# Optimization experiments

Measured on AMD Instinct MI355X. Metric: run time of the kernel, lower is better.

## Reference

```python
import jax, jax.numpy as jnp
import numpy as np
from jax import lax

EPS = 1e-4

@jax.custom_vjp
def bin_active(x):
    # sign binarization with straight-through estimator
    return jnp.sign(x)

def _bin_fwd(x):
    return jnp.sign(x), x

def _bin_bwd(x, g):
    # grad zeroed where input >= 1 or <= -1 (matches torch ge/le)
    return (g * ((x > -1.0) & (x < 1.0)).astype(g.dtype),)

bin_active.defvjp(_bin_fwd, _bin_bwd)

def setup_inputs() -> dict:
    key = jax.random.key(0)
    k1, k2, k3 = jax.random.split(key, 3)
    x = jax.random.normal(k1, (32, 64, 112, 112), dtype=jnp.float32)
    gamma = jnp.ones((64,), dtype=jnp.float32)
    beta = jnp.zeros((64,), dtype=jnp.float32)
    W = jax.random.normal(k2, (64, 64, 3, 3), dtype=jnp.float32) * 0.05
    b = jax.random.normal(k3, (64,), dtype=jnp.float32) * 0.05
    return {"x": x, "gamma": gamma, "beta": beta, "W": W, "b": b}

def reference(x, gamma, beta, W, b):
    # training-mode BatchNorm2d: per-channel batch stats over (N,H,W), biased var
    mean = jnp.mean(x, axis=(0, 2, 3), keepdims=True)
    var = jnp.mean((x - mean) ** 2, axis=(0, 2, 3), keepdims=True)
    xbn = (x - mean) / jnp.sqrt(var + EPS)
    xbn = xbn * gamma.reshape(1, -1, 1, 1) + beta.reshape(1, -1, 1, 1)
    # sign binarize (abs-channel-mean from BinActive is unused downstream)
    xb = bin_active(xbn)
    # conv2d k=3, s=1, p=1
    y = lax.conv_general_dilated(
        xb, W,
        window_strides=(1, 1),
        padding=((1, 1), (1, 1)),
        dimension_numbers=("NCHW", "OIHW", "NCHW"),
    ) + b.reshape(1, -1, 1, 1)
    return jax.nn.relu(y)
```

## Files before the change

kernel.cpp:

```cpp
#include <hip/hip_runtime.h>
#include <stdint.h>

typedef float    f32x4 __attribute__((ext_vector_type(4)));
typedef int      i32x4 __attribute__((ext_vector_type(4)));
typedef uint32_t u32;

#define NHW 401408.0

__device__ __forceinline__ void gload_lds16(const void* g, void* l) {
  typedef __attribute__((address_space(1))) const u32 gu32;
  typedef __attribute__((address_space(3))) u32 lu32;
  __builtin_amdgcn_global_load_lds((gu32*)g, (lu32*)l, 16, 0, 0);
}

__global__ __launch_bounds__(64) void prep_weights(const float* __restrict__ Wg,
                                                   int8_t* __restrict__ Wq,
                                                   float* __restrict__ sc) {
  int o = blockIdx.x, c = threadIdx.x;
  float w[9]; float m = 0.f;
#pragma unroll
  for (int tap = 0; tap < 9; ++tap) {
    w[tap] = Wg[(o * 64 + c) * 9 + tap];
    m = fmaxf(m, fabsf(w[tap]));
  }
#pragma unroll
  for (int off = 32; off > 0; off >>= 1) m = fmaxf(m, __shfl_xor(m, off));
  float s = m / 127.f;
  float inv = (s > 0.f) ? 1.f / s : 0.f;
  if (c == 0) sc[o] = s;
  int of = o >> 4, m16 = o & 15, kg = c >> 4, j = c & 15;
#pragma unroll
  for (int tap = 0; tap < 9; ++tap) {
    int q = (int)rintf(w[tap] * inv);
    q = q > 127 ? 127 : (q < -127 ? -127 : q);
    Wq[(tap * 4 + of) * 1024 + (kg * 16 + m16) * 16 + j] = (int8_t)q;
  }
}

__global__ __launch_bounds__(256) void stats_kernel(const float* __restrict__ x,
                                                    double* __restrict__ sums) {
  int blk = blockIdx.x;
  const float4* p = (const float4*)(x + (size_t)blk * 12544);
  float s = 0.f, q = 0.f;
  for (int i = threadIdx.x; i < 3136; i += 256) {
    float4 v = p[i];
    s += (v.x + v.y) + (v.z + v.w);
    q += v.x * v.x + v.y * v.y + v.z * v.z + v.w * v.w;
  }
#pragma unroll
  for (int off = 32; off > 0; off >>= 1) {
    s += __shfl_down(s, off);
    q += __shfl_down(q, off);
  }
  __shared__ float ls[8];
  int wv = threadIdx.x >> 6;
  if ((threadIdx.x & 63) == 0) { ls[wv] = s; ls[4 + wv] = q; }
  __syncthreads();
  if (threadIdx.x == 0) {
    double S = (double)ls[0] + ls[1] + ls[2] + ls[3];
    double Q = (double)ls[4] + ls[5] + ls[6] + ls[7];
    int c = blk & 63;
    atomicAdd(&sums[c], S);
    atomicAdd(&sums[64 + c], Q);
  }
}

__global__ void finalize_kernel(const double* __restrict__ sums,
                                const float* __restrict__ gamma,
                                const float* __restrict__ beta,
                                float* __restrict__ ad) {
  int c = threadIdx.x;
  double mean = sums[c] / NHW;
  double var  = sums[64 + c] / NHW - mean * mean;
  double istd = 1.0 / sqrt(var + 1e-4);
  double a = (double)gamma[c] * istd;
  double d = (double)beta[c] - mean * a;
  ad[c]      = (float)a;
  ad[64 + c] = (float)d;
}

__global__ __launch_bounds__(256) void binarize_kernel(const float* __restrict__ x,
                                                       const float* __restrict__ ad,
                                                       u32* __restrict__ signs) {
  __shared__ u32 buf[64 * 29];
  const int n = blockIdx.y, h = blockIdx.x, t = threadIdx.x;
  {
    const int c = t & 63, q = t >> 6;
    const float a_c = ad[c], d_c = ad[64 + c];
    const f32x4* src = (const f32x4*)(x + (size_t)(n * 64 + c) * 12544 + h * 112 + q * 28);
#pragma unroll
    for (int i = 0; i < 7; ++i) {
      f32x4 v = src[i];
      u32 p = 0;
#pragma unroll
      for (int k = 0; k < 4; ++k) {
        float tt = fmaf(v[k], a_c, d_c);
        u32 b = (tt > 0.f) ? 0x01u : ((tt < 0.f) ? 0xFFu : 0x00u);
        p |= b << (8 * k);
      }
      buf[c * 29 + q * 7 + i] = p;
    }
  }
  __syncthreads();
  u32* row = signs + (size_t)(n * 112 + h) * 114 * 16;
  const int cq = t & 15, wg = t >> 4;
  if (t < 16) row[t] = 0;
  else if (t < 32) row[113 * 16 + (t - 16)] = 0;
#pragma unroll
  for (int pass = 0; pass < 7; ++pass) {
    int w = wg + 16 * pass;
    int sh = (w & 3) * 8;
    u32 o = 0;
#pragma unroll
    for (int j = 0; j < 4; ++j) {
      u32 v = buf[(cq * 4 + j) * 29 + (w >> 2)];
      o |= ((v >> sh) & 0xFFu) << (8 * j);
    }
    row[(w + 1) * 16 + cq] = o;
  }
}

#define SROW 7296
__global__ __launch_bounds__(256, 2) void conv_kernel(
    const int8_t* __restrict__ signs, const int8_t* __restrict__ Wq,
    const float* __restrict__ sc, const float* __restrict__ bias,
    float* __restrict__ out) {
  __shared__ __align__(16) char smem[6 * SROW];
  const int tid = threadIdx.x, lane = tid & 63, wv = tid >> 6;
  const int b = (blockIdx.x & 7) * 112 + (blockIdx.x >> 3);
  const int n = b / 28, th = b - n * 28;
  const int h0 = th * 4;

  for (int r = wv; r < 6; r += 4) {
    int gh = h0 - 1 + r;
    char* dst = smem + r * SROW;
    if ((unsigned)gh < 112u) {
      const char* g = (const char*)signs + (size_t)(n * 112 + gh) * SROW;
#pragma unroll
      for (int off = 0; off < 7168; off += 1024)
        gload_lds16(g + off + lane * 16, dst + off);
      if (lane < 8) gload_lds16(g + 7168 + lane * 16, dst + 7168);
    } else {
      uint4 z = {0, 0, 0, 0};
      for (int off = lane * 16; off < SROW; off += 1024) *(uint4*)(dst + off) = z;
    }
  }
  __syncthreads();

  i32x4 acc[4][7] = {};
  const int pw = lane & 15, kg = lane >> 4;
#pragma unroll
  for (int tap = 0; tap < 9; ++tap) {
    const int kh = tap / 3, kw = tap - 3 * kh;
    i32x4 af[4], bf[7];
#pragma unroll
    for (int of = 0; of < 4; ++of)
      af[of] = *(const i32x4*)(Wq + (tap * 4 + of) * 1024 + lane * 16);
#pragma unroll
    for (int wf = 0; wf < 7; ++wf)
      bf[wf] = *(const i32x4*)(smem + ((wv + kh) * 114 + wf * 16 + pw + kw) * 64 + kg * 16);
#pragma unroll
    for (int of = 0; of < 4; ++of)
#pragma unroll
      for (int wf = 0; wf < 7; ++wf)
        acc[of][wf] = __builtin_amdgcn_mfma_i32_16x16x64_i8(af[of], bf[wf],
                                                            acc[of][wf], 0, 0, 0);
  }
  __syncthreads();

  float* patch = (float*)smem + wv * (16 * 114);
  const size_t obase = ((size_t)n * 64) * 12544 + (size_t)(h0 + wv) * 112;
#pragma unroll
  for (int of = 0; of < 4; ++of) {
    float sv[4], bv[4];
#pragma unroll
    for (int r = 0; r < 4; ++r) {
      int o = of * 16 + kg * 4 + r;
      sv[r] = sc[o]; bv[r] = bias[o];
    }
#pragma unroll
    for (int wf = 0; wf < 7; ++wf)
#pragma unroll
      for (int r = 0; r < 4; ++r)
        patch[(kg * 4 + r) * 114 + wf * 16 + pw] =
            fmaxf(fmaf((float)acc[of][wf][r], sv[r], bv[r]), 0.f);
    __builtin_amdgcn_s_barrier();
#pragma unroll
    for (int o = 0; o < 16; ++o) {
      float v0 = patch[o * 114 + lane];
      out[obase + (size_t)(of * 16 + o) * 12544 + lane] = v0;
      if (lane < 48) {
        float v1 = patch[o * 114 + 64 + lane];
        out[obase + (size_t)(of * 16 + o) * 12544 + 64 + lane] = v1;
      }
    }
    __builtin_amdgcn_s_barrier();
  }
}

extern "C" void kernel_launch(void* const* d_in, const int* in_sizes, int n_in,
                              void* d_out, int out_size, void* d_ws, size_t ws_size,
                              hipStream_t stream) {
  (void)in_sizes; (void)n_in; (void)out_size; (void)ws_size;
  const float* x     = (const float*)d_in[0];
  const float* gamma = (const float*)d_in[1];
  const float* beta  = (const float*)d_in[2];
  const float* Wg    = (const float*)d_in[3];
  const float* bias  = (const float*)d_in[4];
  float* out = (float*)d_out;

  char* ws = (char*)d_ws;
  float*   ad    = (float*)ws;
  double*  sums  = (double*)(ws + 512);
  float*   sc    = (float*)(ws + 1536);
  int8_t*  Wq    = (int8_t*)(ws + 1792);
  u32*     signs = (u32*)(ws + 38656);

  hipMemsetAsync(sums, 0, 128 * sizeof(double), stream);
  prep_weights<<<dim3(64), dim3(64), 0, stream>>>(Wg, Wq, sc);
  stats_kernel<<<dim3(2048), dim3(256), 0, stream>>>(x, sums);
  finalize_kernel<<<dim3(1), dim3(64), 0, stream>>>(sums, gamma, beta, ad);
  binarize_kernel<<<dim3(112, 32), dim3(256), 0, stream>>>(x, ad, signs);
  conv_kernel<<<dim3(896), dim3(256), 0, stream>>>((const int8_t*)signs, Wq, sc, bias, out);
}
```

Baseline: 248.2 us.

## Split conv output channels across 8 waves and store results directly

Doubles the conv block to 512 threads, with each wave computing half the output channels for one row, which halves the accumulator registers and raises occupancy. The LDS-staged epilogue and its barriers are removed, and results are written directly from MFMA layout to global memory. The intent is better latency hiding and less epilogue synchronisation, at the cost of narrower 64-byte store segments and duplicate B-fragment LDS reads across waves.

```diff
diff --git a/kernel.cpp b/kernel.cpp
--- a/kernel.cpp
+++ b/kernel.cpp
@@ -121,19 +121,21 @@
 }
 
 #define SROW 7296
-__global__ __launch_bounds__(256, 2) void conv_kernel(
+__global__ __launch_bounds__(512, 4) void conv_kernel(
     const int8_t* __restrict__ signs, const int8_t* __restrict__ Wq,
     const float* __restrict__ sc, const float* __restrict__ bias,
     float* __restrict__ out) {
   __shared__ __align__(16) char smem[6 * SROW];
   const int tid = threadIdx.x, lane = tid & 63, wv = tid >> 6;
+  const int r4 = wv & 3;
+  const int p  = wv >> 2;
   const int b = (blockIdx.x & 7) * 112 + (blockIdx.x >> 3);
   const int n = b / 28, th = b - n * 28;
   const int h0 = th * 4;
 
-  for (int r = wv; r < 6; r += 4) {
-    int gh = h0 - 1 + r;
-    char* dst = smem + r * SROW;
+  if (wv < 6) {
+    int gh = h0 - 1 + wv;
+    char* dst = smem + wv * SROW;
     if ((unsigned)gh < 112u) {
       const char* g = (const char*)signs + (size_t)(n * 112 + gh) * SROW;
 #pragma unroll
@@ -147,54 +149,41 @@
   }
   __syncthreads();
 
-  i32x4 acc[4][7] = {};
+  i32x4 acc[2][7] = {};
   const int pw = lane & 15, kg = lane >> 4;
 #pragma unroll
   for (int tap = 0; tap < 9; ++tap) {
     const int kh = tap / 3, kw = tap - 3 * kh;
-    i32x4 af[4], bf[7];
-#pragma unroll
-    for (int of = 0; of < 4; ++of)
-      af[of] = *(const i32x4*)(Wq + (tap * 4 + of) * 1024 + lane * 16);
+    i32x4 af0 = *(const i32x4*)(Wq + (tap * 4 + 2 * p) * 1024 + lane * 16);
+    i32x4 af1 = *(const i32x4*)(Wq + (tap * 4 + 2 * p + 1) * 1024 + lane * 16);
+    i32x4 bf[7];
 #pragma unroll
     for (int wf = 0; wf < 7; ++wf)
-      bf[wf] = *(const i32x4*)(smem + ((wv + kh) * 114 + wf * 16 + pw + kw) * 64 + kg * 16);
-#pragma unroll
-    for (int of = 0; of < 4; ++of)
+      bf[wf] = *(const i32x4*)(smem + ((r4 + kh) * 114 + wf * 16 + pw + kw) * 64 + kg * 16);
+#pragma unroll
+    for (int wf = 0; wf < 7; ++wf) {
+      acc[0][wf] = __builtin_amdgcn_mfma_i32_16x16x64_i8(af0, bf[wf], acc[0][wf], 0, 0, 0);
+      acc[1][wf] = __builtin_amdgcn_mfma_i32_16x16x64_i8(af1, bf[wf], acc[1][wf], 0, 0, 0);
+    }
+  }
+
+  const int h = h0 + r4;
+#pragma unroll
+  for (int i = 0; i < 2; ++i) {
+    float sv[4], bv[4];
+#pragma unroll
+    for (int rr = 0; rr < 4; ++rr) {
+      int o = (2 * p + i) * 16 + kg * 4 + rr;
+      sv[rr] = sc[o]; bv[rr] = bias[o];
+    }
+#pragma unroll
+    for (int rr = 0; rr < 4; ++rr) {
+      int o = (2 * p + i) * 16 + kg * 4 + rr;
+      float* orow = out + ((size_t)(n * 64 + o) * 112 + h) * 112;
 #pragma unroll
       for (int wf = 0; wf < 7; ++wf)
-        acc[of][wf] = __builtin_amdgcn_mfma_i32_16x16x64_i8(af[of], bf[wf],
-                                                            acc[of][wf], 0, 0, 0);
-  }
-  __syncthreads();
-
-  float* patch = (float*)smem + wv * (16 * 114);
-  const size_t obase = ((size_t)n * 64) * 12544 + (size_t)(h0 + wv) * 112;
-#pragma unroll
-  for (int of = 0; of < 4; ++of) {
-    float sv[4], bv[4];
-#pragma unroll
-    for (int r = 0; r < 4; ++r) {
-      int o = of * 16 + kg * 4 + r;
-      sv[r] = sc[o]; bv[r] = bias[o];
-    }
-#pragma unroll
-    for (int wf = 0; wf < 7; ++wf)
-#pragma unroll
-      for (int r = 0; r < 4; ++r)
-        patch[(kg * 4 + r) * 114 + wf * 16 + pw] =
-            fmaxf(fmaf((float)acc[of][wf][r], sv[r], bv[r]), 0.f);
-    __builtin_amdgcn_s_barrier();
-#pragma unroll
-    for (int o = 0; o < 16; ++o) {
-      float v0 = patch[o * 114 + lane];
-      out[obase + (size_t)(of * 16 + o) * 12544 + lane] = v0;
-      if (lane < 48) {
-        float v1 = patch[o * 114 + 64 + lane];
-        out[obase + (size_t)(of * 16 + o) * 12544 + 64 + lane] = v1;
-      }
-    }
-    __builtin_amdgcn_s_barrier();
+        orow[wf * 16 + pw] = fmaxf(fmaf((float)acc[i][wf][rr], sv[rr], bv[rr]), 0.f);
+    }
   }
 }
 
@@ -221,5 +210,5 @@
   stats_kernel<<<dim3(2048), dim3(256), 0, stream>>>(x, sums);
   finalize_kernel<<<dim3(1), dim3(64), 0, stream>>>(sums, gamma, beta, ad);
   binarize_kernel<<<dim3(112, 32), dim3(256), 0, stream>>>(x, ad, signs);
-  conv_kernel<<<dim3(896), dim3(256), 0, stream>>>((const int8_t*)signs, Wq, sc, bias, out);
-}
+  conv_kernel<<<dim3(896), dim3(512), 0, stream>>>((const int8_t*)signs, Wq, sc, bias, out);
+}
```

New measurement: 236.5 us. 4.7% less time.
